# Performance work log

Measured on AMD Instinct MI355X. Metric: run time of the kernel, lower is better.

The kernel has to match this reference:

```python
import jax, jax.numpy as jnp
import numpy as np

B, L, D = 8, 4096, 256
G, K = 64, 8          # n_groups, group_size
N = G * K             # 512 slots
H = 8                 # attention heads
EPS = 1e-5

def _ln(x, g, b):
    m = jnp.mean(x, axis=-1, keepdims=True)
    v = jnp.var(x, axis=-1, keepdims=True)
    return (x - m) * jax.lax.rsqrt(v + EPS) * g + b

def _gelu(x):
    return jax.nn.gelu(x, approximate=False)  # torch nn.GELU default = exact erf

def setup_inputs() -> dict:
    key = jax.random.key(0)
    ks = jax.random.split(key, 24)
    s = 0.02
    d = {
        'X': jax.random.normal(ks[0], (B, L, D), jnp.float32),
        'S': jax.random.normal(ks[1], (B, N, D), jnp.float32),
        'Wg':  jax.random.normal(ks[2], (D, G)) * s,
        'Wk':  jax.random.normal(ks[3], (D, K)) * s,
        'Wm1': jax.random.normal(ks[4], (D, 2*D)) * s, 'bm1': jnp.zeros((2*D,)),
        'Wm2': jax.random.normal(ks[5], (2*D, D)) * s, 'bm2': jnp.zeros((D,)),
        'Wgt1': jax.random.normal(ks[6], (D, D)) * s, 'bgt1': jnp.zeros((D,)),
        'Wgt2': jax.random.normal(ks[7], (D, 1)) * s, 'bgt2': jnp.zeros((1,)),
        'Wqkv': jax.random.normal(ks[8], (D, 3*D)) * s, 'bqkv': jnp.zeros((3*D,)),
        'Wo':  jax.random.normal(ks[9], (D, D)) * s, 'bo': jnp.zeros((D,)),
        'aln_g': jnp.ones((D,)), 'aln_b': jnp.zeros((D,)),
        'Wu1': jax.random.normal(ks[10], (2*D, 2*D)) * s, 'bu1': jnp.zeros((2*D,)),
        'Wu2': jax.random.normal(ks[11], (2*D, D)) * s, 'bu2': jnp.zeros((D,)),
        'ln_g': jnp.ones((D,)), 'ln_b': jnp.zeros((D,)),
    }
    return d

def reference(X, S, Wg, Wk, Wm1, bm1, Wm2, bm2, Wgt1, bgt1, Wgt2, bgt2,
              Wqkv, bqkv, Wo, bo, aln_g, aln_b, Wu1, bu1, Wu2, bu2, ln_g, ln_b):
    # --- hierarchical routing (eval path: argmax one-hot) ---
    msg = _gelu(X @ Wm1 + bm1) @ Wm2 + bm2                 # (B,L,D)
    gate = jax.nn.sigmoid(_gelu(X @ Wgt1 + bgt1) @ Wgt2 + bgt2)  # (B,L,1)
    gm = msg * gate
    gidx = jnp.argmax(X @ Wg, axis=-1)                     # (B,L)
    kidx = jnp.argmax(X @ Wk, axis=-1)                     # (B,L)
    idx = gidx * K + kidx                                  # flat slot id in [0,N)
    full = jax.nn.one_hot(idx, N, dtype=X.dtype)           # (B,L,N)
    incoming = jnp.einsum('bln,bld->bnd', full, gm)        # (B,N,D)
    # --- slot self-attention ---
    qkv = S @ Wqkv + bqkv
    q, k, v = jnp.split(qkv, 3, axis=-1)
    dh = D // H
    q = q.reshape(B, N, H, dh); k = k.reshape(B, N, H, dh); v = v.reshape(B, N, H, dh)
    scores = jnp.einsum('bqhd,bkhd->bhqk', q, k) / jnp.sqrt(jnp.asarray(dh, X.dtype))
    attn = jax.nn.softmax(scores, axis=-1)
    o = jnp.einsum('bhqk,bkhd->bqhd', attn, v).reshape(B, N, D) @ Wo + bo
    S1 = _ln(S + o, aln_g, aln_b)
    # --- update ---
    cat = jnp.concatenate([S1, incoming], axis=-1)         # (B,N,2D)
    S2 = S1 + _gelu(cat @ Wu1 + bu1) @ Wu2 + bu2
    return _ln(S2, ln_g, ln_b)
```

## Files before the change

### kernel.cpp

```cpp
#include <hip/hip_runtime.h>

typedef __bf16 bf16_t;
typedef __bf16 bf16x8 __attribute__((ext_vector_type(8)));
typedef __bf16 bf16x4v __attribute__((ext_vector_type(4)));
typedef __bf16 bf16x2v __attribute__((ext_vector_type(2)));
typedef float f32x4 __attribute__((ext_vector_type(4)));
typedef unsigned long long u64;

#define LN_EPS 1e-5f

__device__ __forceinline__ float erf_fast(float a) {
  const float t = fabsf(a);
  const float s = a * a;
  float r;
  if (t > 0.921875f) {
    float u;
    r = fmaf(-1.72853470e-5f, t, 3.83197126e-4f);
    u = fmaf(-3.88396438e-3f, t, 2.42546219e-2f);
    r = fmaf(r, s, u);
    r = fmaf(r, t, 1.06777877e-1f);
    r = fmaf(r, t, -6.37245935e-1f);
    r = fmaf(r, t, -1.28717512e-1f);
    r = fmaf(r, t, t);
    r = 1.0f - __expf(-r);
    r = copysignf(r, a);
  } else {
    r = -5.96761703e-4f;
    r = fmaf(r, s, 4.99119423e-3f);
    r = fmaf(r, s, -2.67681349e-2f);
    r = fmaf(r, s, 1.12819925e-1f);
    r = fmaf(r, s, -3.76125336e-1f);
    r = fmaf(r, s, 1.28379166e-1f);
    r = fmaf(r, a, a);
  }
  return r;
}

__device__ __forceinline__ float gelu_f(float x) {
  const float h = 0.5f * x;
  return fmaf(h, erf_fast(x * 0.70710678118654752f), h);
}

__device__ __forceinline__ void async16(const bf16_t* g, bf16_t* l) {
  __builtin_amdgcn_global_load_lds(
      (const __attribute__((address_space(1))) void*)g,
      (__attribute__((address_space(3))) void*)l, 16, 0, 0);
}

__global__ __launch_bounds__(256)
void prep_kernel(const float* __restrict__ X, const float* __restrict__ S,
                 const float* __restrict__ Wg, const float* __restrict__ Wk,
                 const float* __restrict__ Wm1, const float* __restrict__ Wgt1,
                 const float* __restrict__ Wm2, const float* __restrict__ Wqkv,
                 const float* __restrict__ Wo, const float* __restrict__ Wu1,
                 const float* __restrict__ Wu2,
                 bf16_t* __restrict__ Xb, bf16_t* __restrict__ Sb,
                 bf16_t* __restrict__ W1t, bf16_t* __restrict__ W2t,
                 bf16_t* __restrict__ Wqkvt, bf16_t* __restrict__ Wot,
                 bf16_t* __restrict__ Wu1t, bf16_t* __restrict__ Wu2t,
                 float4* __restrict__ zbase)
{
  const int bid = blockIdx.x;
  const int t = threadIdx.x;
  if (bid < 8192) {
    const int i = bid * 256 + t;
    const float4 v = ((const float4*)X)[i];
    bf16x4v o; o[0]=(bf16_t)v.x; o[1]=(bf16_t)v.y; o[2]=(bf16_t)v.z; o[3]=(bf16_t)v.w;
    ((bf16x4v*)Xb)[i] = o;
  } else if (bid < 9216) {
    const int i = (bid - 8192) * 256 + t;
    const float4 v = ((const float4*)S)[i];
    bf16x4v o; o[0]=(bf16_t)v.x; o[1]=(bf16_t)v.y; o[2]=(bf16_t)v.z; o[3]=(bf16_t)v.w;
    ((bf16x4v*)Sb)[i] = o;
  } else if (bid < 10112) {
    const int n = bid - 9216;
    const int k = t;
    float v;
    if (n < 512)      v = Wm1[k * 512 + n];
    else if (n < 768) v = Wgt1[k * 256 + (n - 512)];
    else if (n < 832) v = Wg[k * 64 + (n - 768)];
    else if (n < 840) v = Wk[k * 8 + (n - 832)];
    else              v = 0.f;
    W1t[n * 256 + k] = (bf16_t)v;
  } else if (bid < 10368) {
    const int n = bid - 10112;
    for (int k = t; k < 512; k += 256) W2t[n * 512 + k] = (bf16_t)Wm2[k * 256 + n];
  } else if (bid < 11136) {
    const int n = bid - 10368;
    Wqkvt[n * 256 + t] = (bf16_t)Wqkv[t * 768 + n];
  } else if (bid < 11392) {
    const int n = bid - 11136;
    Wot[n * 256 + t] = (bf16_t)Wo[t * 256 + n];
  } else if (bid < 11904) {
    const int n = bid - 11392;
    for (int k = t; k < 512; k += 256) Wu1t[n * 512 + k] = (bf16_t)Wu1[k * 512 + n];
  } else if (bid < 12160) {
    const int n = bid - 11904;
    for (int k = t; k < 512; k += 256) Wu2t[n * 512 + k] = (bf16_t)Wu2[k * 256 + n];
  } else {
    zbase[(bid - 12160) * 256 + t] = make_float4(0.f, 0.f, 0.f, 0.f);
  }
}

__global__ __launch_bounds__(256, 2)
void g1qkv_kernel(const bf16_t* __restrict__ A,
                  const bf16_t* __restrict__ Bt,
                  const float* __restrict__ bias, const float* __restrict__ bias2,
                  bf16_t* __restrict__ h1,
                  const float* __restrict__ wgt2, float* __restrict__ gatelin,
                  u64* __restrict__ bitmap,
                  const bf16_t* __restrict__ Sb, const bf16_t* __restrict__ Wqkvt,
                  const float* __restrict__ bqkv, bf16_t* __restrict__ qkvb,
                  bf16_t* __restrict__ Vt)
{
  const int bid = blockIdx.x;
  const int t = threadIdx.x;
  const int w = t >> 6;
  const int lane = t & 63;
  const int wr = w >> 1, wc = w & 1;
  const int quad = lane >> 4, l15 = lane & 15;

  __shared__ bf16_t lA[128 * 32];
  __shared__ bf16_t lB[128 * 32];
  __shared__ float sWg[256];
  __shared__ int sKi[128];

  if (bid >= 1792) {
    const int id = bid - 1792;
    const int m0 = (id & 63) * 64;
    const int n0 = (id >> 6) * 128;

    f32x4 acc[2][4];
#pragma unroll
    for (int mt = 0; mt < 2; ++mt)
#pragma unroll
      for (int nt = 0; nt < 4; ++nt)
        acc[mt][nt] = (f32x4){0.f, 0.f, 0.f, 0.f};

    for (int k0 = 0; k0 < 256; k0 += 32) {
      async16(Sb + (size_t)(m0 + (t >> 2)) * 256 + k0 + (t & 3) * 8,
              lA + (size_t)(t & 192) * 8);
#pragma unroll
      for (int i = 0; i < 2; ++i) {
        const int c = i * 256 + t;
        async16(Wqkvt + (size_t)(n0 + (c >> 2)) * 256 + k0 + (c & 3) * 8,
                lB + (size_t)(i * 256 + (t & 192)) * 8);
      }
      __syncthreads();
      bf16x8 af[2], bfr[4];
      const int ko = quad * 8;
#pragma unroll
      for (int mt = 0; mt < 2; ++mt)
        af[mt] = *(const bf16x8*)&lA[(wr * 32 + mt * 16 + l15) * 32 + ko];
#pragma unroll
      for (int nt = 0; nt < 4; ++nt)
        bfr[nt] = *(const bf16x8*)&lB[(wc * 64 + nt * 16 + l15) * 32 + ko];
#pragma unroll
      for (int mt = 0; mt < 2; ++mt)
#pragma unroll
        for (int nt = 0; nt < 4; ++nt)
          acc[mt][nt] = __builtin_amdgcn_mfma_f32_16x16x32_bf16(bfr[nt], af[mt], acc[mt][nt], 0, 0, 0);
      __syncthreads();
    }

    if (n0 < 512) {
#pragma unroll
      for (int mt = 0; mt < 2; ++mt) {
        const int row = m0 + wr * 32 + mt * 16 + l15;
#pragma unroll
        for (int nt = 0; nt < 4; ++nt) {
          const int colb = n0 + wc * 64 + nt * 16 + quad * 4;
          const float4 bb = *(const float4*)&bqkv[colb];
          bf16x4v o; o[0]=(bf16_t)(acc[mt][nt][0]+bb.x); o[1]=(bf16_t)(acc[mt][nt][1]+bb.y);
          o[2]=(bf16_t)(acc[mt][nt][2]+bb.z); o[3]=(bf16_t)(acc[mt][nt][3]+bb.w);
          *(bf16x4v*)&qkvb[(size_t)row * 768 + colb] = o;
        }
      }
    } else {
#pragma unroll
      for (int mt = 0; mt < 2; ++mt) {
        const int row = m0 + wr * 32 + mt * 16 + l15;
        const int b = row >> 9, key = row & 511;
#pragma unroll
        for (int nt = 0; nt < 4; ++nt) {
          const int colb = n0 + wc * 64 + nt * 16 + quad * 4;
          const int c = colb - 512;
          const int h2 = c >> 5, dh = c & 31;
          const float4 bb = *(const float4*)&bqkv[colb];
          bf16_t* vb = Vt + ((size_t)(b * 8 + h2) * 32 + dh) * 512 + key;
          vb[0]   = (bf16_t)(acc[mt][nt][0] + bb.x);
          vb[512] = (bf16_t)(acc[mt][nt][1] + bb.y);
          vb[1024]= (bf16_t)(acc[mt][nt][2] + bb.z);
          vb[1536]= (bf16_t)(acc[mt][nt][3] + bb.w);
        }
      }
    }
    return;
  }

  const int m0 = (bid & 255) * 128;
  const int by = bid >> 8;
  const int n0 = by * 128;

  if (by >= 4 && by < 6) sWg[t] = wgt2[t];

  f32x4 acc[4][4];
#pragma unroll
  for (int mt = 0; mt < 4; ++mt)
#pragma unroll
    for (int nt = 0; nt < 4; ++nt)
      acc[mt][nt] = (f32x4){0.f, 0.f, 0.f, 0.f};

  const int srow = t >> 2;
  const int schunk = ((t & 3) ^ (srow & 3)) * 8;
  const int ko = ((quad ^ (l15 & 3)) << 3);

  for (int k0 = 0; k0 < 256; k0 += 32) {
#pragma unroll
    for (int i = 0; i < 2; ++i) {
      const int row = i * 64 + srow;
      async16(A + (size_t)(m0 + row) * 256 + k0 + schunk,
              lA + (size_t)(i * 256 + (t & 192)) * 8);
      async16(Bt + (size_t)(n0 + row) * 256 + k0 + schunk,
              lB + (size_t)(i * 256 + (t & 192)) * 8);
    }
    __syncthreads();
    bf16x8 af[4], bfr[4];
#pragma unroll
    for (int mt = 0; mt < 4; ++mt)
      af[mt] = *(const bf16x8*)&lA[(wr * 64 + mt * 16 + l15) * 32 + ko];
#pragma unroll
    for (int nt = 0; nt < 4; ++nt)
      bfr[nt] = *(const bf16x8*)&lB[(wc * 64 + nt * 16 + l15) * 32 + ko];
#pragma unroll
    for (int mt = 0; mt < 4; ++mt)
#pragma unroll
      for (int nt = 0; nt < 4; ++nt)
        acc[mt][nt] = __builtin_amdgcn_mfma_f32_16x16x32_bf16(bfr[nt], af[mt], acc[mt][nt], 0, 0, 0);
    __syncthreads();
  }

  if (by < 4) {
#pragma unroll
    for (int mt = 0; mt < 4; ++mt) {
      const int row = m0 + wr * 64 + mt * 16 + l15;
#pragma unroll
      for (int nt = 0; nt < 4; ++nt) {
        const int colb = n0 + wc * 64 + nt * 16 + quad * 4;
        const float4 bb = *(const float4*)&bias[colb];
        bf16x4v o;
        o[0] = (bf16_t)gelu_f(acc[mt][nt][0] + bb.x);
        o[1] = (bf16_t)gelu_f(acc[mt][nt][1] + bb.y);
        o[2] = (bf16_t)gelu_f(acc[mt][nt][2] + bb.z);
        o[3] = (bf16_t)gelu_f(acc[mt][nt][3] + bb.w);
        *(bf16x4v*)&h1[(size_t)row * 512 + colb] = o;
      }
    }
  } else if (by < 6) {
#pragma unroll
    for (int mt = 0; mt < 4; ++mt) {
      const int row = m0 + wr * 64 + mt * 16 + l15;
      float part = 0.f;
#pragma unroll
      for (int nt = 0; nt < 4; ++nt) {
        const int colb = n0 + wc * 64 + nt * 16 + quad * 4;
        const int c = colb - 512;
        const float4 bb = *(const float4*)&bias2[c];
        part = fmaf(gelu_f(acc[mt][nt][0] + bb.x), sWg[c + 0], part);
        part = fmaf(gelu_f(acc[mt][nt][1] + bb.y), sWg[c + 1], part);
        part = fmaf(gelu_f(acc[mt][nt][2] + bb.z), sWg[c + 2], part);
        part = fmaf(gelu_f(acc[mt][nt][3] + bb.w), sWg[c + 3], part);
      }
      part += __shfl_xor(part, 16, 64);
      part += __shfl_xor(part, 32, 64);
      if (lane < 16) atomicAdd(&gatelin[row], part);
    }
  } else {
    int bi[4];
#pragma unroll
    for (int mt = 0; mt < 4; ++mt) {
      if (wc == 0) {
        float mv = -1e30f; int mi = 0;
#pragma unroll
        for (int nt = 0; nt < 4; ++nt)
#pragma unroll
          for (int j = 0; j < 4; ++j) {
            const int gc = nt * 16 + quad * 4 + j;
            const float v = acc[mt][nt][j];
            if (v > mv || (v == mv && gc < mi)) { mv = v; mi = gc; }
          }
#pragma unroll
        for (int off = 16; off <= 32; off <<= 1) {
          const float ov = __shfl_xor(mv, off, 64);
          const int oi = __shfl_xor(mi, off, 64);
          if (ov > mv || (ov == mv && oi < mi)) { mv = ov; mi = oi; }
        }
        bi[mt] = mi;
      } else {
        float mv = -1e30f; int mi = 0;
        if (quad < 2) {
#pragma unroll
          for (int j = 0; j < 4; ++j) {
            const int kc = quad * 4 + j;
            const float v = acc[mt][0][j];
            if (v > mv || (v == mv && kc < mi)) { mv = v; mi = kc; }
          }
        }
#pragma unroll
        for (int off = 16; off <= 32; off <<= 1) {
          const float ov = __shfl_xor(mv, off, 64);
          const int oi = __shfl_xor(mi, off, 64);
          if (ov > mv || (ov == mv && oi < mi)) { mv = ov; mi = oi; }
        }
        if (lane < 16) sKi[wr * 64 + mt * 16 + l15] = mi;
      }
    }
    __syncthreads();
    if (wc == 0 && lane < 16) {
#pragma unroll
      for (int mt = 0; mt < 4; ++mt) {
        const int rl = wr * 64 + mt * 16 + l15;
        const int row = m0 + rl;
        const int idx = bi[mt] * 8 + sKi[rl];
        const int b = row >> 12, tok = row & 4095;
        atomicOr(&bitmap[(size_t)(b * 512 + idx) * 64 + (tok >> 6)],
                 1ull << (tok & 63));
      }
    }
  }
}

template<int MT, int EPI>
__global__ __launch_bounds__(256)
void gemm_kernel(const bf16_t* __restrict__ A, int lda,
                 const bf16_t* __restrict__ Bt, int K,
                 const float* __restrict__ bias, const float* __restrict__ bias2,
                 void* __restrict__ outp, int ldc,
                 const float* __restrict__ wgt2, float* __restrict__ gatelin,
                 u64* __restrict__ bitmap)
{
  constexpr int BM = MT * 32;
  constexpr int CA = BM * 4;
  const int m0 = blockIdx.x * BM;
  const int by = blockIdx.y;
  const int n0 = by * 128;
  const int t = threadIdx.x;
  const int w = t >> 6;
  const int lane = t & 63;
  const int wr = w >> 1, wc = w & 1;
  const int quad = lane >> 4, l15 = lane & 15;

  __shared__ bf16_t lA[BM * 32];
  __shared__ bf16_t lB[128 * 32];

  f32x4 acc[MT][4];
#pragma unroll
  for (int mt = 0; mt < MT; ++mt)
#pragma unroll
    for (int nt = 0; nt < 4; ++nt)
      acc[mt][nt] = (f32x4){0.f, 0.f, 0.f, 0.f};

  for (int k0 = 0; k0 < K; k0 += 32) {
    if constexpr (CA >= 256) {
#pragma unroll
      for (int i = 0; i < CA / 256; ++i) {
        const int c = i * 256 + t;
        async16(A + (size_t)(m0 + (c >> 2)) * lda + k0 + (c & 3) * 8,
                lA + (size_t)(i * 256 + (t & 192)) * 8);
      }
    } else {
      if (t < CA)
        async16(A + (size_t)(m0 + (t >> 2)) * lda + k0 + (t & 3) * 8,
                lA + (size_t)(t & 192) * 8);
    }
#pragma unroll
    for (int i = 0; i < 2; ++i) {
      const int c = i * 256 + t;
      async16(Bt + (size_t)(n0 + (c >> 2)) * K + k0 + (c & 3) * 8,
              lB + (size_t)(i * 256 + (t & 192)) * 8);
    }
    __syncthreads();
    bf16x8 af[MT], bfr[4];
    const int ko = quad * 8;
#pragma unroll
    for (int mt = 0; mt < MT; ++mt)
      af[mt] = *(const bf16x8*)&lA[(wr * MT * 16 + mt * 16 + l15) * 32 + ko];
#pragma unroll
    for (int nt = 0; nt < 4; ++nt)
      bfr[nt] = *(const bf16x8*)&lB[(wc * 64 + nt * 16 + l15) * 32 + ko];
#pragma unroll
    for (int mt = 0; mt < MT; ++mt)
#pragma unroll
      for (int nt = 0; nt < 4; ++nt)
        acc[mt][nt] = __builtin_amdgcn_mfma_f32_16x16x32_bf16(bfr[nt], af[mt], acc[mt][nt], 0, 0, 0);
    __syncthreads();
  }

#pragma unroll
  for (int mt = 0; mt < MT; ++mt) {
    const int row = m0 + wr * MT * 16 + mt * 16 + l15;
#pragma unroll
    for (int nt = 0; nt < 4; ++nt) {
      const int colb = n0 + wc * 64 + nt * 16 + quad * 4;
      const float4 bb = *(const float4*)&bias[colb];
      bf16x4v o;
      o[0]=(bf16_t)gelu_f(acc[mt][nt][0]+bb.x); o[1]=(bf16_t)gelu_f(acc[mt][nt][1]+bb.y);
      o[2]=(bf16_t)gelu_f(acc[mt][nt][2]+bb.z); o[3]=(bf16_t)gelu_f(acc[mt][nt][3]+bb.w);
      *(bf16x4v*)&((bf16_t*)outp)[(size_t)row * ldc + colb] = o;
    }
  }
  (void)bias2; (void)wgt2; (void)gatelin; (void)bitmap;
}

__global__ __launch_bounds__(256)
void gather_kernel(const bf16_t* __restrict__ h1, const float* __restrict__ gatelin,
                   const float* __restrict__ bgt2, const u64* __restrict__ bitmap,
                   bf16_t* __restrict__ H, float* __restrict__ sumg)
{
  const int bs = blockIdx.x;
  const int b = bs >> 9;
  const int t = threadIdx.x;
  __shared__ u64 sw[64];
  if (t < 64) sw[t] = bitmap[(size_t)bs * 64 + t];
  __syncthreads();
  const float bg = bgt2[0];
  float a0 = 0.f, a1 = 0.f, sg = 0.f;
  for (int wd = 0; wd < 64; ++wd) {
    u64 word = sw[wd];
    while (word) {
      const int bit = __builtin_ctzll(word);
      word &= word - 1;
      const int l = (b << 12) + (wd << 6) + bit;
      const float g = 1.0f / (1.0f + __expf(-(gatelin[l] + bg)));
      const bf16x2v hv = *(const bf16x2v*)&h1[(size_t)l * 512 + t * 2];
      a0 = fmaf(g, (float)hv[0], a0);
      a1 = fmaf(g, (float)hv[1], a1);
      sg += g;
    }
  }
  bf16x2v o; o[0] = (bf16_t)a0; o[1] = (bf16_t)a1;
  *(bf16x2v*)&H[(size_t)bs * 512 + t * 2] = o;
  if (t == 0) sumg[bs] = sg;
}

__global__ __launch_bounds__(256)
void g2attn_kernel(const bf16_t* __restrict__ qkv, const bf16_t* __restrict__ Vt,
                   bf16_t* __restrict__ obuf,
                   const bf16_t* __restrict__ H, const bf16_t* __restrict__ W2t,
                   const float* __restrict__ bm2, const float* __restrict__ sumg,
                   float* __restrict__ incom)
{
  const int bid = blockIdx.x;
  const int t = threadIdx.x;
  const int w = t >> 6, lane = t & 63;
  const int quad = lane >> 4, l15 = lane & 15;

  __shared__ bf16_t sP[32 * 520];
  __shared__ float sL[32];

  if (bid < 128) {
    const int wr = w >> 1, wc = w & 1;
    const int m0 = (bid & 63) * 64;
    const int n0 = (bid >> 6) * 128;
    bf16_t* lA = sP;
    bf16_t* lB = sP + 64 * 32;

    f32x4 acc[2][4];
#pragma unroll
    for (int mt = 0; mt < 2; ++mt)
#pragma unroll
      for (int nt = 0; nt < 4; ++nt)
        acc[mt][nt] = (f32x4){0.f, 0.f, 0.f, 0.f};

    for (int k0 = 0; k0 < 512; k0 += 32) {
      async16(H + (size_t)(m0 + (t >> 2)) * 512 + k0 + (t & 3) * 8,
              lA + (size_t)(t & 192) * 8);
#pragma unroll
      for (int i = 0; i < 2; ++i) {
        const int c = i * 256 + t;
        async16(W2t + (size_t)(n0 + (c >> 2)) * 512 + k0 + (c & 3) * 8,
                lB + (size_t)(i * 256 + (t & 192)) * 8);
      }
      __syncthreads();
      bf16x8 af[2], bfr[4];
      const int ko = quad * 8;
#pragma unroll
      for (int mt = 0; mt < 2; ++mt)
        af[mt] = *(const bf16x8*)&lA[(wr * 32 + mt * 16 + l15) * 32 + ko];
#pragma unroll
      for (int nt = 0; nt < 4; ++nt)
        bfr[nt] = *(const bf16x8*)&lB[(wc * 64 + nt * 16 + l15) * 32 + ko];
#pragma unroll
      for (int mt = 0; mt < 2; ++mt)
#pragma unroll
        for (int nt = 0; nt < 4; ++nt)
          acc[mt][nt] = __builtin_amdgcn_mfma_f32_16x16x32_bf16(bfr[nt], af[mt], acc[mt][nt], 0, 0, 0);
      __syncthreads();
    }

#pragma unroll
    for (int mt = 0; mt < 2; ++mt) {
      const int row = m0 + wr * 32 + mt * 16 + l15;
      const float gt = sumg[row];
#pragma unroll
      for (int nt = 0; nt < 4; ++nt) {
        const int colb = n0 + wc * 64 + nt * 16 + quad * 4;
        const float4 bb = *(const float4*)&bm2[colb];
        *(float4*)&incom[(size_t)row * 256 + colb] =
            make_float4(fmaf(gt, bb.x, acc[mt][nt][0]), fmaf(gt, bb.y, acc[mt][nt][1]),
                        fmaf(gt, bb.z, acc[mt][nt][2]), fmaf(gt, bb.w, acc[mt][nt][3]));
      }
    }
    return;
  }

  const int abid = bid - 128;
  const int qc = abid & 15;
  const int h = (abid >> 4) & 7;
  const int b = abid >> 7;

  bf16x8 qf[2];
#pragma unroll
  for (int mt = 0; mt < 2; ++mt) {
    const int row = b * 512 + qc * 32 + mt * 16 + l15;
    qf[mt] = *(const bf16x8*)&qkv[(size_t)row * 768 + h * 32 + quad * 8];
  }
  const float scale = 0.17677669529663687f;
  for (int kt = w; kt < 32; kt += 4) {
    const int key = b * 512 + kt * 16 + l15;
    const bf16x8 kf = *(const bf16x8*)&qkv[(size_t)key * 768 + 256 + h * 32 + quad * 8];
#pragma unroll
    for (int mt = 0; mt < 2; ++mt) {
      f32x4 c = (f32x4){0.f, 0.f, 0.f, 0.f};
      c = __builtin_amdgcn_mfma_f32_16x16x32_bf16(qf[mt], kf, c, 0, 0, 0);
#pragma unroll
      for (int r = 0; r < 4; ++r)
        sP[(mt * 16 + quad * 4 + r) * 520 + kt * 16 + l15] = (bf16_t)(c[r] * scale);
    }
  }
  __syncthreads();

#pragma unroll
  for (int ri = 0; ri < 8; ++ri) {
    const int row = w * 8 + ri;
    const bf16x8 sv = *(const bf16x8*)&sP[row * 520 + lane * 8];
    float sval[8];
    float mx = -1e30f;
#pragma unroll
    for (int j = 0; j < 8; ++j) { sval[j] = (float)sv[j]; mx = fmaxf(mx, sval[j]); }
#pragma unroll
    for (int off = 32; off; off >>= 1) mx = fmaxf(mx, __shfl_xor(mx, off, 64));
    float sum = 0.f;
    bf16x8 pv;
#pragma unroll
    for (int j = 0; j < 8; ++j) { const float e = __expf(sval[j] - mx); sum += e; pv[j] = (bf16_t)e; }
#pragma unroll
    for (int off = 32; off; off >>= 1) sum += __shfl_xor(sum, off, 64);
    *(bf16x8*)&sP[row * 520 + lane * 8] = pv;
    if (lane == 0) sL[row] = sum;
  }
  __syncthreads();

  const int wq = w >> 1, wd = w & 1;
  const bf16_t* vbase = Vt + ((size_t)(b * 8 + h) * 32 + wd * 16 + l15) * 512;
  const bf16_t* pbase = &sP[(wq * 16 + l15) * 520];
  f32x4 oacc = (f32x4){0.f, 0.f, 0.f, 0.f};
#pragma unroll
  for (int kt = 0; kt < 16; ++kt) {
    const bf16x8 af = *(const bf16x8*)&pbase[kt * 32 + quad * 8];
    const bf16x8 vf = *(const bf16x8*)&vbase[kt * 32 + quad * 8];
    oacc = __builtin_amdgcn_mfma_f32_16x16x32_bf16(vf, af, oacc, 0, 0, 0);
  }
  const int rowq = wq * 16 + l15;
  const float inv = 1.0f / sL[rowq];
  bf16x4v o;
#pragma unroll
  for (int r = 0; r < 4; ++r) o[r] = (bf16_t)(oacc[r] * inv);
  *(bf16x4v*)&obuf[(size_t)(b * 512 + qc * 32 + rowq) * 256 + h * 32 + wd * 16 + quad * 4] = o;
}

__global__ __launch_bounds__(256)
void wo_ln1_kernel(const bf16_t* __restrict__ obuf, const bf16_t* __restrict__ Wot,
                   const float* __restrict__ bo, const float* __restrict__ S,
                   const float* __restrict__ incom, const float* __restrict__ g,
                   const float* __restrict__ bb, float* __restrict__ S1f,
                   bf16_t* __restrict__ A4)
{
  const int m0 = blockIdx.x * 16;
  const int t = threadIdx.x;
  const int w = t >> 6, lane = t & 63;
  const int quad = lane >> 4, l15 = lane & 15;

  __shared__ bf16_t lA[16 * 32];
  __shared__ bf16_t lB[256 * 32];
  __shared__ float sSum[4][16];
  __shared__ float sSq[4][16];

  f32x4 acc[4];
#pragma unroll
  for (int nt = 0; nt < 4; ++nt) acc[nt] = (f32x4){0.f, 0.f, 0.f, 0.f};

  for (int k0 = 0; k0 < 256; k0 += 32) {
    if (t < 64)
      async16(obuf + (size_t)(m0 + (t >> 2)) * 256 + k0 + (t & 3) * 8, lA);
#pragma unroll
    for (int i = 0; i < 4; ++i) {
      const int c = i * 256 + t;
      async16(Wot + (size_t)(c >> 2) * 256 + k0 + (c & 3) * 8,
              lB + (size_t)(i * 256 + (t & 192)) * 8);
    }
    __syncthreads();
    const int ko = quad * 8;
    const bf16x8 af = *(const bf16x8*)&lA[l15 * 32 + ko];
#pragma unroll
    for (int nt = 0; nt < 4; ++nt) {
      const bf16x8 bfr = *(const bf16x8*)&lB[(w * 64 + nt * 16 + l15) * 32 + ko];
      acc[nt] = __builtin_amdgcn_mfma_f32_16x16x32_bf16(bfr, af, acc[nt], 0, 0, 0);
    }
    __syncthreads();
  }

  const int row = m0 + l15;
  float sum = 0.f, sq = 0.f;
#pragma unroll
  for (int nt = 0; nt < 4; ++nt) {
    const int colb = w * 64 + nt * 16 + quad * 4;
    const float4 bv = *(const float4*)&bo[colb];
    const float4 sv = *(const float4*)&S[(size_t)row * 256 + colb];
    float x0 = acc[nt][0] + bv.x + sv.x, x1 = acc[nt][1] + bv.y + sv.y;
    float x2 = acc[nt][2] + bv.z + sv.z, x3 = acc[nt][3] + bv.w + sv.w;
    acc[nt][0] = x0; acc[nt][1] = x1; acc[nt][2] = x2; acc[nt][3] = x3;
    sum += x0 + x1 + x2 + x3;
    sq += x0*x0 + x1*x1 + x2*x2 + x3*x3;
  }
  sum += __shfl_xor(sum, 16, 64); sum += __shfl_xor(sum, 32, 64);
  sq  += __shfl_xor(sq, 16, 64);  sq  += __shfl_xor(sq, 32, 64);
  if (lane < 16) { sSum[w][l15] = sum; sSq[w][l15] = sq; }
  __syncthreads();
  const float tot = sSum[0][l15] + sSum[1][l15] + sSum[2][l15] + sSum[3][l15];
  const float tq  = sSq[0][l15] + sSq[1][l15] + sSq[2][l15] + sSq[3][l15];
  const float mean = tot * 0.00390625f;
  const float var = tq * 0.00390625f - mean * mean;
  const float rstd = rsqrtf(var + LN_EPS);
#pragma unroll
  for (int nt = 0; nt < 4; ++nt) {
    const int colb = w * 64 + nt * 16 + quad * 4;
    const float4 gg = *(const float4*)&g[colb];
    const float4 bv = *(const float4*)&bb[colb];
    const float y0 = (acc[nt][0]-mean)*rstd*gg.x + bv.x;
    const float y1 = (acc[nt][1]-mean)*rstd*gg.y + bv.y;
    const float y2 = (acc[nt][2]-mean)*rstd*gg.z + bv.z;
    const float y3 = (acc[nt][3]-mean)*rstd*gg.w + bv.w;
    *(float4*)&S1f[(size_t)row * 256 + colb] = make_float4(y0, y1, y2, y3);
    bf16x4v yb; yb[0]=(bf16_t)y0; yb[1]=(bf16_t)y1; yb[2]=(bf16_t)y2; yb[3]=(bf16_t)y3;
    *(bf16x4v*)&A4[(size_t)row * 512 + colb] = yb;
    const float4 ic = *(const float4*)&incom[(size_t)row * 256 + colb];
    bf16x4v ib; ib[0]=(bf16_t)ic.x; ib[1]=(bf16_t)ic.y; ib[2]=(bf16_t)ic.z; ib[3]=(bf16_t)ic.w;
    *(bf16x4v*)&A4[(size_t)row * 512 + 256 + colb] = ib;
  }
}

__global__ __launch_bounds__(256)
void wu2_ln2_kernel(const bf16_t* __restrict__ U, const bf16_t* __restrict__ Wu2t,
                    const float* __restrict__ bu2, const float* __restrict__ S1f,
                    const float* __restrict__ g, const float* __restrict__ bb,
                    float* __restrict__ out)
{
  const int m0 = blockIdx.x * 16;
  const int t = threadIdx.x;
  const int w = t >> 6, lane = t & 63;
  const int quad = lane >> 4, l15 = lane & 15;

  __shared__ bf16_t lA[16 * 32];
  __shared__ bf16_t lB[256 * 32];
  __shared__ float sSum[4][16];
  __shared__ float sSq[4][16];

  f32x4 acc[4];
#pragma unroll
  for (int nt = 0; nt < 4; ++nt) acc[nt] = (f32x4){0.f, 0.f, 0.f, 0.f};

  for (int k0 = 0; k0 < 512; k0 += 32) {
    if (t < 64)
      async16(U + (size_t)(m0 + (t >> 2)) * 512 + k0 + (t & 3) * 8, lA);
#pragma unroll
    for (int i = 0; i < 4; ++i) {
      const int c = i * 256 + t;
      async16(Wu2t + (size_t)(c >> 2) * 512 + k0 + (c & 3) * 8,
              lB + (size_t)(i * 256 + (t & 192)) * 8);
    }
    __syncthreads();
    const int ko = quad * 8;
    const bf16x8 af = *(const bf16x8*)&lA[l15 * 32 + ko];
#pragma unroll
    for (int nt = 0; nt < 4; ++nt) {
      const bf16x8 bfr = *(const bf16x8*)&lB[(w * 64 + nt * 16 + l15) * 32 + ko];
      acc[nt] = __builtin_amdgcn_mfma_f32_16x16x32_bf16(bfr, af, acc[nt], 0, 0, 0);
    }
    __syncthreads();
  }

  const int row = m0 + l15;
  float sum = 0.f, sq = 0.f;
#pragma unroll
  for (int nt = 0; nt < 4; ++nt) {
    const int colb = w * 64 + nt * 16 + quad * 4;
    const float4 bv = *(const float4*)&bu2[colb];
    const float4 sv = *(const float4*)&S1f[(size_t)row * 256 + colb];
    float x0 = acc[nt][0] + bv.x + sv.x, x1 = acc[nt][1] + bv.y + sv.y;
    float x2 = acc[nt][2] + bv.z + sv.z, x3 = acc[nt][3] + bv.w + sv.w;
    acc[nt][0] = x0; acc[nt][1] = x1; acc[nt][2] = x2; acc[nt][3] = x3;
    sum += x0 + x1 + x2 + x3;
    sq += x0*x0 + x1*x1 + x2*x2 + x3*x3;
  }
  sum += __shfl_xor(sum, 16, 64); sum += __shfl_xor(sum, 32, 64);
  sq  += __shfl_xor(sq, 16, 64);  sq  += __shfl_xor(sq, 32, 64);
  if (lane < 16) { sSum[w][l15] = sum; sSq[w][l15] = sq; }
  __syncthreads();
  const float tot = sSum[0][l15] + sSum[1][l15] + sSum[2][l15] + sSum[3][l15];
  const float tq  = sSq[0][l15] + sSq[1][l15] + sSq[2][l15] + sSq[3][l15];
  const float mean = tot * 0.00390625f;
  const float var = tq * 0.00390625f - mean * mean;
  const float rstd = rsqrtf(var + LN_EPS);
#pragma unroll
  for (int nt = 0; nt < 4; ++nt) {
    const int colb = w * 64 + nt * 16 + quad * 4;
    const float4 gg = *(const float4*)&g[colb];
    const float4 bv = *(const float4*)&bb[colb];
    *(float4*)&out[(size_t)row * 256 + colb] = make_float4(
        (acc[nt][0]-mean)*rstd*gg.x + bv.x, (acc[nt][1]-mean)*rstd*gg.y + bv.y,
        (acc[nt][2]-mean)*rstd*gg.z + bv.z, (acc[nt][3]-mean)*rstd*gg.w + bv.w);
  }
}

extern "C" void kernel_launch(void* const* d_in, const int* in_sizes, int n_in,
                              void* d_out, int out_size, void* d_ws, size_t ws_size,
                              hipStream_t stream)
{
  (void)in_sizes; (void)n_in; (void)out_size; (void)ws_size;
  const float* X    = (const float*)d_in[0];
  const float* S    = (const float*)d_in[1];
  const float* Wg   = (const float*)d_in[2];
  const float* Wk   = (const float*)d_in[3];
  const float* Wm1  = (const float*)d_in[4];
  const float* bm1  = (const float*)d_in[5];
  const float* Wm2  = (const float*)d_in[6];
  const float* bm2  = (const float*)d_in[7];
  const float* Wgt1 = (const float*)d_in[8];
  const float* bgt1 = (const float*)d_in[9];
  const float* Wgt2 = (const float*)d_in[10];
  const float* bgt2 = (const float*)d_in[11];
  const float* Wqkv = (const float*)d_in[12];
  const float* bqkv = (const float*)d_in[13];
  const float* Wo   = (const float*)d_in[14];
  const float* bo   = (const float*)d_in[15];
  const float* alng = (const float*)d_in[16];
  const float* alnb = (const float*)d_in[17];
  const float* Wu1  = (const float*)d_in[18];
  const float* bu1  = (const float*)d_in[19];
  const float* Wu2  = (const float*)d_in[20];
  const float* bu2  = (const float*)d_in[21];
  const float* lng  = (const float*)d_in[22];
  const float* lnb  = (const float*)d_in[23];

  char* p = (char*)d_ws;
  auto carve = [&](size_t bytes) { char* r = p; p += bytes; return r; };
  bf16_t* Xb    = (bf16_t*)carve(16777216);
  bf16_t* Sb    = (bf16_t*)carve(2097152);
  bf16_t* W1t   = (bf16_t*)carve(458752);
  bf16_t* W2t   = (bf16_t*)carve(262144);
  bf16_t* Wqkvt = (bf16_t*)carve(393216);
  bf16_t* Wot   = (bf16_t*)carve(131072);
  bf16_t* Wu1t  = (bf16_t*)carve(524288);
  bf16_t* Wu2t  = (bf16_t*)carve(262144);
  bf16_t* h1    = (bf16_t*)carve(33554432);
  u64*    bitmap  = (u64*)carve(2097152);
  float*  gatelin = (float*)carve(131072);
  float*  incom = (float*)carve(4194304);
  bf16_t* qkvb  = (bf16_t*)carve(6291456);
  bf16_t* Vt    = (bf16_t*)carve(2097152);
  bf16_t* obuf  = (bf16_t*)carve(2097152);
  float*  S1f   = (float*)carve(4194304);
  bf16_t* A4    = (bf16_t*)carve(4194304);
  bf16_t* U     = (bf16_t*)carve(4194304);
  float*  sumg  = (float*)carve(16384);
  bf16_t* H = U;

  prep_kernel<<<12704, 256, 0, stream>>>(X, S, Wg, Wk, Wm1, Wgt1, Wm2, Wqkv, Wo, Wu1, Wu2,
                                         Xb, Sb, W1t, W2t, Wqkvt, Wot, Wu1t, Wu2t,
                                         (float4*)bitmap);
  g1qkv_kernel<<<2176, 256, 0, stream>>>(Xb, W1t, bm1, bgt1, h1,
                                         Wgt2, gatelin, bitmap,
                                         Sb, Wqkvt, bqkv, qkvb, Vt);
  gather_kernel<<<4096, 256, 0, stream>>>(h1, gatelin, bgt2, bitmap, H, sumg);
  g2attn_kernel<<<1152, 256, 0, stream>>>(qkvb, Vt, obuf,
                                          H, W2t, bm2, sumg, incom);
  wo_ln1_kernel<<<256, 256, 0, stream>>>(obuf, Wot, bo, S, incom, alng, alnb, S1f, A4);
  gemm_kernel<2,5><<<dim3(64,4), 256, 0, stream>>>(A4, 512, Wu1t, 512, bu1, nullptr, U, 512,
                                                   nullptr, nullptr, nullptr);
  wu2_ln2_kernel<<<256, 256, 0, stream>>>(U, Wu2t, bu2, S1f, lng, lnb, (float*)d_out);
}
```

Before: 249.1 us.

## Fuse Wo+LN1, Wu1 GEMM and Wu2+LN2 into one tail kernel

Merges three tail kernels into one. Each 16-row block now computes the Wo projection and first LayerNorm, then the Wu1 GEMM with GELU, then the Wu2 GEMM and final LayerNorm. Intermediates (S1, the concatenated input and U) stay in LDS instead of round-tripping through global memory, which removes two launches and the S1f, A4 and U buffers. It also XOR-swizzles the weight chunks in LDS to reduce bank conflicts. The costs are that every block streams the full Wu1 and Wu2 weights, the Wu1 stage runs on only 256 blocks, and the residual S1 is now reread in bf16 rather than fp32.

```diff
diff --git a/kernel.cpp b/kernel.cpp
--- a/kernel.cpp
+++ b/kernel.cpp
@@ -330,88 +330,6 @@
   }
 }
 
-template<int MT, int EPI>
-__global__ __launch_bounds__(256)
-void gemm_kernel(const bf16_t* __restrict__ A, int lda,
-                 const bf16_t* __restrict__ Bt, int K,
-                 const float* __restrict__ bias, const float* __restrict__ bias2,
-                 void* __restrict__ outp, int ldc,
-                 const float* __restrict__ wgt2, float* __restrict__ gatelin,
-                 u64* __restrict__ bitmap)
-{
-  constexpr int BM = MT * 32;
-  constexpr int CA = BM * 4;
-  const int m0 = blockIdx.x * BM;
-  const int by = blockIdx.y;
-  const int n0 = by * 128;
-  const int t = threadIdx.x;
-  const int w = t >> 6;
-  const int lane = t & 63;
-  const int wr = w >> 1, wc = w & 1;
-  const int quad = lane >> 4, l15 = lane & 15;
-
-  __shared__ bf16_t lA[BM * 32];
-  __shared__ bf16_t lB[128 * 32];
-
-  f32x4 acc[MT][4];
-#pragma unroll
-  for (int mt = 0; mt < MT; ++mt)
-#pragma unroll
-    for (int nt = 0; nt < 4; ++nt)
-      acc[mt][nt] = (f32x4){0.f, 0.f, 0.f, 0.f};
-
-  for (int k0 = 0; k0 < K; k0 += 32) {
-    if constexpr (CA >= 256) {
-#pragma unroll
-      for (int i = 0; i < CA / 256; ++i) {
-        const int c = i * 256 + t;
-        async16(A + (size_t)(m0 + (c >> 2)) * lda + k0 + (c & 3) * 8,
-                lA + (size_t)(i * 256 + (t & 192)) * 8);
-      }
-    } else {
-      if (t < CA)
-        async16(A + (size_t)(m0 + (t >> 2)) * lda + k0 + (t & 3) * 8,
-                lA + (size_t)(t & 192) * 8);
-    }
-#pragma unroll
-    for (int i = 0; i < 2; ++i) {
-      const int c = i * 256 + t;
-      async16(Bt + (size_t)(n0 + (c >> 2)) * K + k0 + (c & 3) * 8,
-              lB + (size_t)(i * 256 + (t & 192)) * 8);
-    }
-    __syncthreads();
-    bf16x8 af[MT], bfr[4];
-    const int ko = quad * 8;
-#pragma unroll
-    for (int mt = 0; mt < MT; ++mt)
-      af[mt] = *(const bf16x8*)&lA[(wr * MT * 16 + mt * 16 + l15) * 32 + ko];
-#pragma unroll
-    for (int nt = 0; nt < 4; ++nt)
-      bfr[nt] = *(const bf16x8*)&lB[(wc * 64 + nt * 16 + l15) * 32 + ko];
-#pragma unroll
-    for (int mt = 0; mt < MT; ++mt)
-#pragma unroll
-      for (int nt = 0; nt < 4; ++nt)
-        acc[mt][nt] = __builtin_amdgcn_mfma_f32_16x16x32_bf16(bfr[nt], af[mt], acc[mt][nt], 0, 0, 0);
-    __syncthreads();
-  }
-
-#pragma unroll
-  for (int mt = 0; mt < MT; ++mt) {
-    const int row = m0 + wr * MT * 16 + mt * 16 + l15;
-#pragma unroll
-    for (int nt = 0; nt < 4; ++nt) {
-      const int colb = n0 + wc * 64 + nt * 16 + quad * 4;
-      const float4 bb = *(const float4*)&bias[colb];
-      bf16x4v o;
-      o[0]=(bf16_t)gelu_f(acc[mt][nt][0]+bb.x); o[1]=(bf16_t)gelu_f(acc[mt][nt][1]+bb.y);
-      o[2]=(bf16_t)gelu_f(acc[mt][nt][2]+bb.z); o[3]=(bf16_t)gelu_f(acc[mt][nt][3]+bb.w);
-      *(bf16x4v*)&((bf16_t*)outp)[(size_t)row * ldc + colb] = o;
-    }
-  }
-  (void)bias2; (void)wgt2; (void)gatelin; (void)bitmap;
-}
-
 __global__ __launch_bounds__(256)
 void gather_kernel(const bf16_t* __restrict__ h1, const float* __restrict__ gatelin,
                    const float* __restrict__ bgt2, const u64* __restrict__ bitmap,
@@ -580,156 +498,185 @@
 }
 
 __global__ __launch_bounds__(256)
-void wo_ln1_kernel(const bf16_t* __restrict__ obuf, const bf16_t* __restrict__ Wot,
-                   const float* __restrict__ bo, const float* __restrict__ S,
-                   const float* __restrict__ incom, const float* __restrict__ g,
-                   const float* __restrict__ bb, float* __restrict__ S1f,
-                   bf16_t* __restrict__ A4)
+void tail_kernel(const bf16_t* __restrict__ obuf, const bf16_t* __restrict__ Wot,
+                 const float* __restrict__ bo, const float* __restrict__ S,
+                 const float* __restrict__ incom,
+                 const float* __restrict__ g1n, const float* __restrict__ b1n,
+                 const bf16_t* __restrict__ Wu1t, const float* __restrict__ bu1,
+                 const bf16_t* __restrict__ Wu2t, const float* __restrict__ bu2,
+                 const float* __restrict__ g2n, const float* __restrict__ b2n,
+                 float* __restrict__ out)
 {
   const int m0 = blockIdx.x * 16;
   const int t = threadIdx.x;
   const int w = t >> 6, lane = t & 63;
   const int quad = lane >> 4, l15 = lane & 15;
 
+  __shared__ bf16_t lB[512 * 32];
   __shared__ bf16_t lA[16 * 32];
-  __shared__ bf16_t lB[256 * 32];
+  __shared__ bf16_t A4s[16 * 520];
+  __shared__ bf16_t Us[16 * 520];
   __shared__ float sSum[4][16];
   __shared__ float sSq[4][16];
 
-  f32x4 acc[4];
-#pragma unroll
-  for (int nt = 0; nt < 4; ++nt) acc[nt] = (f32x4){0.f, 0.f, 0.f, 0.f};
-
-  for (int k0 = 0; k0 < 256; k0 += 32) {
-    if (t < 64)
-      async16(obuf + (size_t)(m0 + (t >> 2)) * 256 + k0 + (t & 3) * 8, lA);
-#pragma unroll
-    for (int i = 0; i < 4; ++i) {
-      const int c = i * 256 + t;
-      async16(Wot + (size_t)(c >> 2) * 256 + k0 + (c & 3) * 8,
-              lB + (size_t)(i * 256 + (t & 192)) * 8);
-    }
+  const int schunk = ((t & 3) ^ ((t >> 2) & 3)) * 8;
+  const int ko_b = ((quad ^ (l15 & 3)) << 3);
+  const int ko_a = quad * 8;
+  const int row = m0 + l15;
+
+  {
+    f32x4 acc[4];
+#pragma unroll
+    for (int nt = 0; nt < 4; ++nt) acc[nt] = (f32x4){0.f, 0.f, 0.f, 0.f};
+
+    for (int k0 = 0; k0 < 256; k0 += 32) {
+      if (t < 64)
+        async16(obuf + (size_t)(m0 + (t >> 2)) * 256 + k0 + (t & 3) * 8, lA);
+#pragma unroll
+      for (int i = 0; i < 4; ++i) {
+        const int c = i * 256 + t;
+        async16(Wot + (size_t)(c >> 2) * 256 + k0 + schunk,
+                lB + (size_t)(i * 256 + (t & 192)) * 8);
+      }
+      __syncthreads();
+      const bf16x8 af = *(const bf16x8*)&lA[l15 * 32 + ko_a];
+#pragma unroll
+      for (int nt = 0; nt < 4; ++nt) {
+        const bf16x8 bfr = *(const bf16x8*)&lB[(w * 64 + nt * 16 + l15) * 32 + ko_b];
+        acc[nt] = __builtin_amdgcn_mfma_f32_16x16x32_bf16(bfr, af, acc[nt], 0, 0, 0);
+      }
+      __syncthreads();
+    }
+
+    float sum = 0.f, sq = 0.f;
+#pragma unroll
+    for (int nt = 0; nt < 4; ++nt) {
+      const int colb = w * 64 + nt * 16 + quad * 4;
+      const float4 bv = *(const float4*)&bo[colb];
+      const float4 sv = *(const float4*)&S[(size_t)row * 256 + colb];
+      float x0 = acc[nt][0] + bv.x + sv.x, x1 = acc[nt][1] + bv.y + sv.y;
+      float x2 = acc[nt][2] + bv.z + sv.z, x3 = acc[nt][3] + bv.w + sv.w;
+      acc[nt][0] = x0; acc[nt][1] = x1; acc[nt][2] = x2; acc[nt][3] = x3;
+      sum += x0 + x1 + x2 + x3;
+      sq += x0*x0 + x1*x1 + x2*x2 + x3*x3;
+    }
+    sum += __shfl_xor(sum, 16, 64); sum += __shfl_xor(sum, 32, 64);
+    sq  += __shfl_xor(sq, 16, 64);  sq  += __shfl_xor(sq, 32, 64);
+    if (lane < 16) { sSum[w][l15] = sum; sSq[w][l15] = sq; }
     __syncthreads();
-    const int ko = quad * 8;
-    const bf16x8 af = *(const bf16x8*)&lA[l15 * 32 + ko];
+    const float tot = sSum[0][l15] + sSum[1][l15] + sSum[2][l15] + sSum[3][l15];
+    const float tq  = sSq[0][l15] + sSq[1][l15] + sSq[2][l15] + sSq[3][l15];
+    const float mean = tot * 0.00390625f;
+    const float var = tq * 0.00390625f - mean * mean;
+    const float rstd = rsqrtf(var + LN_EPS);
 #pragma unroll
     for (int nt = 0; nt < 4; ++nt) {
-      const bf16x8 bfr = *(const bf16x8*)&lB[(w * 64 + nt * 16 + l15) * 32 + ko];
-      acc[nt] = __builtin_amdgcn_mfma_f32_16x16x32_bf16(bfr, af, acc[nt], 0, 0, 0);
-    }
+      const int colb = w * 64 + nt * 16 + quad * 4;
+      const float4 gg = *(const float4*)&g1n[colb];
+      const float4 bv = *(const float4*)&b1n[colb];
+      bf16x4v yb;
+      yb[0] = (bf16_t)((acc[nt][0]-mean)*rstd*gg.x + bv.x);
+      yb[1] = (bf16_t)((acc[nt][1]-mean)*rstd*gg.y + bv.y);
+      yb[2] = (bf16_t)((acc[nt][2]-mean)*rstd*gg.z + bv.z);
+      yb[3] = (bf16_t)((acc[nt][3]-mean)*rstd*gg.w + bv.w);
+      *(bf16x4v*)&A4s[l15 * 520 + colb] = yb;
+      const float4 ic = *(const float4*)&incom[(size_t)row * 256 + colb];
+      bf16x4v ib; ib[0]=(bf16_t)ic.x; ib[1]=(bf16_t)ic.y; ib[2]=(bf16_t)ic.z; ib[3]=(bf16_t)ic.w;
+      *(bf16x4v*)&A4s[l15 * 520 + 256 + colb] = ib;
+    }
+  }
+  __syncthreads();
+
+  {
+    f32x4 acc2[8];
+#pragma unroll
+    for (int nt = 0; nt < 8; ++nt) acc2[nt] = (f32x4){0.f, 0.f, 0.f, 0.f};
+
+    for (int k0 = 0; k0 < 512; k0 += 32) {
+#pragma unroll
+      for (int i = 0; i < 8; ++i) {
+        const int c = i * 256 + t;
+        async16(Wu1t + (size_t)(c >> 2) * 512 + k0 + schunk,
+                lB + (size_t)(i * 256 + (t & 192)) * 8);
+      }
+      __syncthreads();
+      const bf16x8 af = *(const bf16x8*)&A4s[l15 * 520 + k0 + ko_a];
+#pragma unroll
+      for (int nt = 0; nt < 8; ++nt) {
+        const bf16x8 bfr = *(const bf16x8*)&lB[(w * 128 + nt * 16 + l15) * 32 + ko_b];
+        acc2[nt] = __builtin_amdgcn_mfma_f32_16x16x32_bf16(bfr, af, acc2[nt], 0, 0, 0);
+      }
+      __syncthreads();
+    }
+#pragma unroll
+    for (int nt = 0; nt < 8; ++nt) {
+      const int colb = w * 128 + nt * 16 + quad * 4;
+      const float4 bb = *(const float4*)&bu1[colb];
+      bf16x4v o;
+      o[0] = (bf16_t)gelu_f(acc2[nt][0] + bb.x);
+      o[1] = (bf16_t)gelu_f(acc2[nt][1] + bb.y);
+      o[2] = (bf16_t)gelu_f(acc2[nt][2] + bb.z);
+      o[3] = (bf16_t)gelu_f(acc2[nt][3] + bb.w);
+      *(bf16x4v*)&Us[l15 * 520 + colb] = o;
+    }
+  }
+  __syncthreads();
+
+  {
+    f32x4 acc3[4];
+#pragma unroll
+    for (int nt = 0; nt < 4; ++nt) acc3[nt] = (f32x4){0.f, 0.f, 0.f, 0.f};
+
+    for (int k0 = 0; k0 < 512; k0 += 32) {
+#pragma unroll
+      for (int i = 0; i < 4; ++i) {
+        const int c = i * 256 + t;
+        async16(Wu2t + (size_t)(c >> 2) * 512 + k0 + schunk,
+                lB + (size_t)(i * 256 + (t & 192)) * 8);
+      }
+      __syncthreads();
+      const bf16x8 af = *(const bf16x8*)&Us[l15 * 520 + k0 + ko_a];
+#pragma unroll
+      for (int nt = 0; nt < 4; ++nt) {
+        const bf16x8 bfr = *(const bf16x8*)&lB[(w * 64 + nt * 16 + l15) * 32 + ko_b];
+        acc3[nt] = __builtin_amdgcn_mfma_f32_16x16x32_bf16(bfr, af, acc3[nt], 0, 0, 0);
+      }
+      __syncthreads();
+    }
+
+    float sum = 0.f, sq = 0.f;
+#pragma unroll
+    for (int nt = 0; nt < 4; ++nt) {
+      const int colb = w * 64 + nt * 16 + quad * 4;
+      const float4 bv = *(const float4*)&bu2[colb];
+      const bf16x4v s1v = *(const bf16x4v*)&A4s[l15 * 520 + colb];
+      float x0 = acc3[nt][0] + bv.x + (float)s1v[0];
+      float x1 = acc3[nt][1] + bv.y + (float)s1v[1];
+      float x2 = acc3[nt][2] + bv.z + (float)s1v[2];
+      float x3 = acc3[nt][3] + bv.w + (float)s1v[3];
+      acc3[nt][0] = x0; acc3[nt][1] = x1; acc3[nt][2] = x2; acc3[nt][3] = x3;
+      sum += x0 + x1 + x2 + x3;
+      sq += x0*x0 + x1*x1 + x2*x2 + x3*x3;
+    }
+    sum += __shfl_xor(sum, 16, 64); sum += __shfl_xor(sum, 32, 64);
+    sq  += __shfl_xor(sq, 16, 64);  sq  += __shfl_xor(sq, 32, 64);
     __syncthreads();
-  }
-
-  const int row = m0 + l15;
-  float sum = 0.f, sq = 0.f;
-#pragma unroll
-  for (int nt = 0; nt < 4; ++nt) {
-    const int colb = w * 64 + nt * 16 + quad * 4;
-    const float4 bv = *(const float4*)&bo[colb];
-    const float4 sv = *(const float4*)&S[(size_t)row * 256 + colb];
-    float x0 = acc[nt][0] + bv.x + sv.x, x1 = acc[nt][1] + bv.y + sv.y;
-    float x2 = acc[nt][2] + bv.z + sv.z, x3 = acc[nt][3] + bv.w + sv.w;
-    acc[nt][0] = x0; acc[nt][1] = x1; acc[nt][2] = x2; acc[nt][3] = x3;
-    sum += x0 + x1 + x2 + x3;
-    sq += x0*x0 + x1*x1 + x2*x2 + x3*x3;
-  }
-  sum += __shfl_xor(sum, 16, 64); sum += __shfl_xor(sum, 32, 64);
-  sq  += __shfl_xor(sq, 16, 64);  sq  += __shfl_xor(sq, 32, 64);
-  if (lane < 16) { sSum[w][l15] = sum; sSq[w][l15] = sq; }
-  __syncthreads();
-  const float tot = sSum[0][l15] + sSum[1][l15] + sSum[2][l15] + sSum[3][l15];
-  const float tq  = sSq[0][l15] + sSq[1][l15] + sSq[2][l15] + sSq[3][l15];
-  const float mean = tot * 0.00390625f;
-  const float var = tq * 0.00390625f - mean * mean;
-  const float rstd = rsqrtf(var + LN_EPS);
-#pragma unroll
-  for (int nt = 0; nt < 4; ++nt) {
-    const int colb = w * 64 + nt * 16 + quad * 4;
-    const float4 gg = *(const float4*)&g[colb];
-    const float4 bv = *(const float4*)&bb[colb];
-    const float y0 = (acc[nt][0]-mean)*rstd*gg.x + bv.x;
-    const float y1 = (acc[nt][1]-mean)*rstd*gg.y + bv.y;
-    const float y2 = (acc[nt][2]-mean)*rstd*gg.z + bv.z;
-    const float y3 = (acc[nt][3]-mean)*rstd*gg.w + bv.w;
-    *(float4*)&S1f[(size_t)row * 256 + colb] = make_float4(y0, y1, y2, y3);
-    bf16x4v yb; yb[0]=(bf16_t)y0; yb[1]=(bf16_t)y1; yb[2]=(bf16_t)y2; yb[3]=(bf16_t)y3;
-    *(bf16x4v*)&A4[(size_t)row * 512 + colb] = yb;
-    const float4 ic = *(const float4*)&incom[(size_t)row * 256 + colb];
-    bf16x4v ib; ib[0]=(bf16_t)ic.x; ib[1]=(bf16_t)ic.y; ib[2]=(bf16_t)ic.z; ib[3]=(bf16_t)ic.w;
-    *(bf16x4v*)&A4[(size_t)row * 512 + 256 + colb] = ib;
-  }
-}
-
-__global__ __launch_bounds__(256)
-void wu2_ln2_kernel(const bf16_t* __restrict__ U, const bf16_t* __restrict__ Wu2t,
-                    const float* __restrict__ bu2, const float* __restrict__ S1f,
-                    const float* __restrict__ g, const float* __restrict__ bb,
-                    float* __restrict__ out)
-{
-  const int m0 = blockIdx.x * 16;
-  const int t = threadIdx.x;
-  const int w = t >> 6, lane = t & 63;
-  const int quad = lane >> 4, l15 = lane & 15;
-
-  __shared__ bf16_t lA[16 * 32];
-  __shared__ bf16_t lB[256 * 32];
-  __shared__ float sSum[4][16];
-  __shared__ float sSq[4][16];
-
-  f32x4 acc[4];
-#pragma unroll
-  for (int nt = 0; nt < 4; ++nt) acc[nt] = (f32x4){0.f, 0.f, 0.f, 0.f};
-
-  for (int k0 = 0; k0 < 512; k0 += 32) {
-    if (t < 64)
-      async16(U + (size_t)(m0 + (t >> 2)) * 512 + k0 + (t & 3) * 8, lA);
-#pragma unroll
-    for (int i = 0; i < 4; ++i) {
-      const int c = i * 256 + t;
-      async16(Wu2t + (size_t)(c >> 2) * 512 + k0 + (c & 3) * 8,
-              lB + (size_t)(i * 256 + (t & 192)) * 8);
-    }
+    if (lane < 16) { sSum[w][l15] = sum; sSq[w][l15] = sq; }
     __syncthreads();
-    const int ko = quad * 8;
-    const bf16x8 af = *(const bf16x8*)&lA[l15 * 32 + ko];
+    const float tot = sSum[0][l15] + sSum[1][l15] + sSum[2][l15] + sSum[3][l15];
+    const float tq  = sSq[0][l15] + sSq[1][l15] + sSq[2][l15] + sSq[3][l15];
+    const float mean = tot * 0.00390625f;
+    const float var = tq * 0.00390625f - mean * mean;
+    const float rstd = rsqrtf(var + LN_EPS);
 #pragma unroll
     for (int nt = 0; nt < 4; ++nt) {
-      const bf16x8 bfr = *(const bf16x8*)&lB[(w * 64 + nt * 16 + l15) * 32 + ko];
-      acc[nt] = __builtin_amdgcn_mfma_f32_16x16x32_bf16(bfr, af, acc[nt], 0, 0, 0);
-    }
-    __syncthreads();
-  }
-
-  const int row = m0 + l15;
-  float sum = 0.f, sq = 0.f;
-#pragma unroll
-  for (int nt = 0; nt < 4; ++nt) {
-    const int colb = w * 64 + nt * 16 + quad * 4;
-    const float4 bv = *(const float4*)&bu2[colb];
-    const float4 sv = *(const float4*)&S1f[(size_t)row * 256 + colb];
-    float x0 = acc[nt][0] + bv.x + sv.x, x1 = acc[nt][1] + bv.y + sv.y;
-    float x2 = acc[nt][2] + bv.z + sv.z, x3 = acc[nt][3] + bv.w + sv.w;
-    acc[nt][0] = x0; acc[nt][1] = x1; acc[nt][2] = x2; acc[nt][3] = x3;
-    sum += x0 + x1 + x2 + x3;
-    sq += x0*x0 + x1*x1 + x2*x2 + x3*x3;
-  }
-  sum += __shfl_xor(sum, 16, 64); sum += __shfl_xor(sum, 32, 64);
-  sq  += __shfl_xor(sq, 16, 64);  sq  += __shfl_xor(sq, 32, 64);
-  if (lane < 16) { sSum[w][l15] = sum; sSq[w][l15] = sq; }
-  __syncthreads();
-  const float tot = sSum[0][l15] + sSum[1][l15] + sSum[2][l15] + sSum[3][l15];
-  const float tq  = sSq[0][l15] + sSq[1][l15] + sSq[2][l15] + sSq[3][l15];
-  const float mean = tot * 0.00390625f;
-  const float var = tq * 0.00390625f - mean * mean;
-  const float rstd = rsqrtf(var + LN_EPS);
-#pragma unroll
-  for (int nt = 0; nt < 4; ++nt) {
-    const int colb = w * 64 + nt * 16 + quad * 4;
-    const float4 gg = *(const float4*)&g[colb];
-    const float4 bv = *(const float4*)&bb[colb];
-    *(float4*)&out[(size_t)row * 256 + colb] = make_float4(
-        (acc[nt][0]-mean)*rstd*gg.x + bv.x, (acc[nt][1]-mean)*rstd*gg.y + bv.y,
-        (acc[nt][2]-mean)*rstd*gg.z + bv.z, (acc[nt][3]-mean)*rstd*gg.w + bv.w);
+      const int colb = w * 64 + nt * 16 + quad * 4;
+      const float4 gg = *(const float4*)&g2n[colb];
+      const float4 bv = *(const float4*)&b2n[colb];
+      *(float4*)&out[(size_t)row * 256 + colb] = make_float4(
+          (acc3[nt][0]-mean)*rstd*gg.x + bv.x, (acc3[nt][1]-mean)*rstd*gg.y + bv.y,
+          (acc3[nt][2]-mean)*rstd*gg.z + bv.z, (acc3[nt][3]-mean)*rstd*gg.w + bv.w);
+    }
   }
 }
 
@@ -780,11 +727,8 @@
   bf16_t* qkvb  = (bf16_t*)carve(6291456);
   bf16_t* Vt    = (bf16_t*)carve(2097152);
   bf16_t* obuf  = (bf16_t*)carve(2097152);
-  float*  S1f   = (float*)carve(4194304);
-  bf16_t* A4    = (bf16_t*)carve(4194304);
-  bf16_t* U     = (bf16_t*)carve(4194304);
+  bf16_t* H     = (bf16_t*)carve(4194304);
   float*  sumg  = (float*)carve(16384);
-  bf16_t* H = U;
 
   prep_kernel<<<12704, 256, 0, stream>>>(X, S, Wg, Wk, Wm1, Wgt1, Wm2, Wqkv, Wo, Wu1, Wu2,
                                          Xb, Sb, W1t, W2t, Wqkvt, Wot, Wu1t, Wu2t,
@@ -795,8 +739,7 @@
   gather_kernel<<<4096, 256, 0, stream>>>(h1, gatelin, bgt2, bitmap, H, sumg);
   g2attn_kernel<<<1152, 256, 0, stream>>>(qkvb, Vt, obuf,
                                           H, W2t, bm2, sumg, incom);
-  wo_ln1_kernel<<<256, 256, 0, stream>>>(obuf, Wot, bo, S, incom, alng, alnb, S1f, A4);
-  gemm_kernel<2,5><<<dim3(64,4), 256, 0, stream>>>(A4, 512, Wu1t, 512, bu1, nullptr, U, 512,
-                                                   nullptr, nullptr, nullptr);
-  wu2_ln2_kernel<<<256, 256, 0, stream>>>(U, Wu2t, bu2, S1f, lng, lnb, (float*)d_out);
-}
+  tail_kernel<<<256, 256, 0, stream>>>(obuf, Wot, bo, S, incom, alng, alnb,
+                                       Wu1t, bu1, Wu2t, bu2, lng, lnb,
+                                       (float*)d_out);
+}
```

New measurement: 248.6 us. About the same (-0.2%).
